# Performance work log

Hardware: AMD Instinct MI355X
Metric: run time of the kernel (lower is better)

## Reference

```python
import jax, jax.numpy as jnp
import numpy as np

N, E, B = 10000, 60000, 4
NODE_IN, EDGE_IN, COND_IN, SCALE_IN = 6, 6, 10, 4
H, KW, OUT = 64, 256, 1
NUM_LAYERS = 3


def _lin(key, fan_in, fan_out):
    return jax.random.normal(key, (fan_in, fan_out), jnp.float32) / np.sqrt(fan_in).astype(np.float32)


def setup_inputs() -> dict:
    key = jax.random.key(0)
    ks = jax.random.split(key, 16)
    return {
        "x": jax.random.normal(ks[0], (N, NODE_IN), jnp.float32),
        "edge_attr": jax.random.normal(ks[1], (E, EDGE_IN), jnp.float32),
        "conditions": jax.random.normal(ks[2], (B, COND_IN), jnp.float32),
        "scale": jax.random.normal(ks[3], (B, SCALE_IN), jnp.float32),
        "edge_index": jax.random.randint(ks[4], (2, E), 0, N, dtype=jnp.int32),
        "batch": jnp.sort(jax.random.randint(ks[5], (N,), 0, B, dtype=jnp.int32)),
        # node encoder
        "nW1": _lin(ks[6], NODE_IN, H), "nb1": jnp.zeros((H,), jnp.float32),
        "nW2": _lin(ks[7], H, H), "nb2": jnp.zeros((H,), jnp.float32),
        # condition encoder
        "cW1": _lin(ks[8], COND_IN + SCALE_IN, H), "cb1": jnp.zeros((H,), jnp.float32),
        "cW2": _lin(ks[9], H, H), "cb2": jnp.zeros((H,), jnp.float32),
        # kernel network (DenseNet [EDGE_IN+H, KW//2, KW, H*H])
        "kW1": _lin(ks[10], EDGE_IN + H, KW // 2), "kb1": jnp.zeros((KW // 2,), jnp.float32),
        "kW2": _lin(ks[11], KW // 2, KW), "kb2": jnp.zeros((KW,), jnp.float32),
        "kW3": _lin(ks[12], KW, H * H), "kb3": jnp.zeros((H * H,), jnp.float32),
        # NNConv root weight + bias
        "root": _lin(ks[13], H, H), "conv_bias": jnp.zeros((H,), jnp.float32),
        # output head
        "oW": _lin(ks[14], H, OUT), "ob": jnp.zeros((OUT,), jnp.float32),
    }


def reference(x, edge_attr, conditions, scale, edge_index, batch,
              nW1, nb1, nW2, nb2, cW1, cb1, cW2, cb2,
              kW1, kb1, kW2, kb2, kW3, kb3, root, conv_bias, oW, ob):
    # node + condition encoders
    h = jax.nn.relu(x @ nW1 + nb1) @ nW2 + nb2                                   # [N,H]
    u = jax.nn.relu(jnp.concatenate([conditions, scale], 1) @ cW1 + cb1) @ cW2 + cb2  # [B,H]

    src, dst = edge_index[0], edge_index[1]
    # per-edge conditioned attributes
    ea = jnp.concatenate([edge_attr, u[batch[src]]], axis=1)                     # [E,EDGE_IN+H]
    # kernel network -> per-edge H x H weight (same every layer, compute once)
    k = jax.nn.relu(ea @ kW1 + kb1)
    k = jax.nn.relu(k @ kW2 + kb2)
    w = (k @ kW3 + kb3).reshape(E, H, H)                                          # [E,H,H]

    # mean-aggregation degree (clamped to >=1, matching scatter_mean semantics)
    deg = jnp.maximum(jax.ops.segment_sum(jnp.ones((E,), x.dtype), dst, num_segments=N), 1.0)

    for _ in range(NUM_LAYERS):
        msg = jnp.einsum('ei,eio->eo', h[src], w)                                 # gather + bmm
        agg = jax.ops.segment_sum(msg, dst, num_segments=N) / deg[:, None]        # scatter-mean
        h = jax.nn.relu(agg + h @ root + conv_bias)

    out = h @ oW + ob                                                             # [N,OUT]
    return out, u
```

## Files before the change

kernel.cpp:

```cpp
#include <hip/hip_runtime.h>
#include <hip/hip_fp16.h>

#define N_NODES 10000
#define N_EDGES 60000
#define EPAD    60032

typedef _Float16 f16;
typedef f16 f16x8 __attribute__((ext_vector_type(8)));
typedef float f32x4 __attribute__((ext_vector_type(4)));

__global__ void k_node_enc(const float* __restrict__ x, const float* __restrict__ W1,
                           const float* __restrict__ b1, const float* __restrict__ W2,
                           const float* __restrict__ b2, float* __restrict__ h) {
    __shared__ float t[4][64];
    int g = threadIdx.x >> 6, j = threadIdx.x & 63;
    int node = blockIdx.x * 4 + g;
    float acc = b1[j];
#pragma unroll
    for (int i = 0; i < 6; ++i) acc += x[node * 6 + i] * W1[i * 64 + j];
    t[g][j] = fmaxf(acc, 0.f);
    __syncthreads();
    float acc2 = b2[j];
#pragma unroll
    for (int i = 0; i < 64; ++i) acc2 += t[g][i] * W2[i * 64 + j];
    h[node * 64 + j] = acc2;
}

__global__ void k_cond_enc(const float* __restrict__ cond, const float* __restrict__ scl,
                           const float* __restrict__ W1, const float* __restrict__ b1,
                           const float* __restrict__ W2, const float* __restrict__ b2,
                           float* __restrict__ u, float* __restrict__ out_u) {
    __shared__ float t[4][64];
    __shared__ float cat[4][14];
    int g = threadIdx.x >> 6, j = threadIdx.x & 63;
    if (threadIdx.x < 56) {
        int b = threadIdx.x / 14, i = threadIdx.x % 14;
        cat[b][i] = (i < 10) ? cond[b * 10 + i] : scl[b * 4 + (i - 10)];
    }
    __syncthreads();
    float acc = b1[j];
#pragma unroll
    for (int i = 0; i < 14; ++i) acc += cat[g][i] * W1[i * 64 + j];
    t[g][j] = fmaxf(acc, 0.f);
    __syncthreads();
    float acc2 = b2[j];
#pragma unroll
    for (int i = 0; i < 64; ++i) acc2 += t[g][i] * W2[i * 64 + j];
    u[g * 64 + j] = acc2;
    out_u[g * 64 + j] = acc2;
}

__global__ void k_deg(const int* __restrict__ dst, float* __restrict__ deg) {
    int e = blockIdx.x * 256 + threadIdx.x;
    if (e < N_EDGES) atomicAdd(&deg[dst[e]], 1.0f);
}
__global__ void k_deg_inv(float* __restrict__ deg) {
    int n = blockIdx.x * 256 + threadIdx.x;
    if (n < N_NODES) deg[n] = 1.0f / fmaxf(deg[n], 1.0f);
}

__global__ void k_permute(const float* __restrict__ kW3, const float* __restrict__ kb3,
                          f16* __restrict__ kW3P, float* __restrict__ kb3P) {
    __shared__ float T[256][65];
    int i = blockIdx.x;
    int o = threadIdx.x & 63, kq = threadIdx.x >> 6;
    for (int kk = 0; kk < 64; ++kk) {
        int k = kk * 4 + kq;
        T[k][o] = kW3[(size_t)k * 4096 + i * 64 + o];
    }
    if (threadIdx.x < 64) kb3P[threadIdx.x * 64 + i] = kb3[i * 64 + threadIdx.x];
    __syncthreads();
    int ow = threadIdx.x >> 2, kc = (threadIdx.x & 3) * 64;
    f16* dstp = kW3P + (size_t)(ow * 64 + i) * 256 + kc;
    for (int c = 0; c < 8; ++c) {
        f16x8 v;
#pragma unroll
        for (int jj = 0; jj < 8; ++jj) v[jj] = (f16)T[kc + c * 8 + jj][ow];
        *(f16x8*)(dstp + c * 8) = v;
    }
}

__global__ __launch_bounds__(256) void k_edge12(const float* __restrict__ ea, const int* __restrict__ ei,
                                                const int* __restrict__ batch, const float* __restrict__ u,
                                                const float* __restrict__ W1, const float* __restrict__ b1,
                                                const float* __restrict__ W2, const float* __restrict__ b2,
                                                f16* __restrict__ k2) {
    __shared__ float u_s[256];
    __shared__ float ea_s[16][6];
    __shared__ int b_s[16];
    __shared__ float k1_s[16][128];
    int tid = threadIdx.x;
    int e0 = blockIdx.x * 16;
    u_s[tid] = u[tid];
    if (tid < 96) {
        int e = tid / 6, i = tid % 6;
        int eg = e0 + e;
        ea_s[e][i] = (eg < N_EDGES) ? ea[(size_t)eg * 6 + i] : 0.f;
    }
    if (tid < 16) {
        int eg = e0 + tid;
        b_s[tid] = (eg < N_EDGES) ? batch[ei[eg]] : 0;
    }
    __syncthreads();
    int j = tid & 127;
#pragma unroll 1
    for (int p = 0; p < 8; ++p) {
        int e = p * 2 + (tid >> 7);
        float acc = b1[j];
#pragma unroll
        for (int i = 0; i < 6; ++i) acc += ea_s[e][i] * W1[i * 128 + j];
        const float* ur = u_s + b_s[e] * 64;
#pragma unroll
        for (int i = 0; i < 64; ++i) acc += ur[i] * W1[(6 + i) * 128 + j];
        k1_s[e][j] = fmaxf(acc, 0.f);
    }
    __syncthreads();
    float acc2[16];
#pragma unroll
    for (int e = 0; e < 16; ++e) acc2[e] = b2[tid];
    for (int i = 0; i < 128; ++i) {
        float w = W2[(size_t)i * 256 + tid];
#pragma unroll
        for (int e = 0; e < 16; ++e) acc2[e] += k1_s[e][i] * w;
    }
#pragma unroll
    for (int e = 0; e < 16; ++e) {
        int eg = e0 + e;
        k2[(size_t)eg * 256 + tid] = (f16)((eg < N_EDGES) ? fmaxf(acc2[e], 0.f) : 0.f);
    }
}

__global__ __launch_bounds__(256) void k_fused(const f16* __restrict__ A, const f16* __restrict__ Bm,
                                               const float* __restrict__ kb3P, const float* __restrict__ h,
                                               const int* __restrict__ ei, const float* __restrict__ dinv,
                                               float* __restrict__ agg) {
    __shared__ __align__(16) char lB[32768];
    __shared__ int src_s[128];
    __shared__ int dst_s[128];
    __shared__ float dinv_s[128];
    int tid = threadIdx.x, wave = tid >> 6, lane = tid & 63;
    int m0 = blockIdx.x * 128;
    if (tid < 128) {
        int eg = m0 + tid; int s = 0, d = 0; float dv = 0.f;
        if (eg < N_EDGES) { s = ei[eg]; d = ei[N_EDGES + eg]; dv = dinv[d]; }
        src_s[tid] = s; dst_s[tid] = d; dinv_s[tid] = dv;
    }
    __syncthreads();
    f16x8 a[2][8];
#pragma unroll
    for (int mf = 0; mf < 2; ++mf) {
        const f16* ap = A + (size_t)(m0 + wave * 32 + mf * 16 + (lane & 15)) * 256 + (lane >> 4) * 8;
#pragma unroll
        for (int ks = 0; ks < 8; ++ks) a[mf][ks] = *(const f16x8*)(ap + ks * 32);
    }
    float hsr[2][4][4];
#pragma unroll
    for (int mf = 0; mf < 2; ++mf)
#pragma unroll
        for (int jj = 0; jj < 4; ++jj) {
            int el = wave * 32 + mf * 16 + (lane >> 4) * 4 + jj;
            const float* hp = h + (size_t)src_s[el] * 64 + (lane & 15);
            float dv = dinv_s[el];
#pragma unroll
            for (int nf = 0; nf < 4; ++nf) hsr[mf][jj][nf] = hp[nf * 16] * dv;
        }
    int swz = (lane & 7) << 4;
    int rbase = (lane & 15) * 512;
    int koff = (lane >> 4) * 16;
#pragma unroll 1
    for (int ct = 0; ct < 64; ++ct) {
        f16x8 st[8];
        const f16* bp = Bm + (size_t)ct * 64 * 256;
#pragma unroll
        for (int q = 0; q < 8; ++q) {
            int idx = q * 4096 + tid * 16;
            int r = idx >> 9, cb = idx & 511;
            st[q] = *(const f16x8*)(bp + r * 256 + (cb >> 1));
        }
        __syncthreads();
#pragma unroll
        for (int q = 0; q < 8; ++q) {
            int idx = q * 4096 + tid * 16;
            int r = idx >> 9, cb = idx & 511;
            *(f16x8*)(lB + r * 512 + (cb ^ ((r & 7) << 4))) = st[q];
        }
        __syncthreads();
        f32x4 acc[2][4];
#pragma unroll
        for (int nf = 0; nf < 4; ++nf) {
            float bv = kb3P[ct * 64 + nf * 16 + (lane & 15)];
            acc[0][nf] = {bv, bv, bv, bv};
            acc[1][nf] = {bv, bv, bv, bv};
        }
#pragma unroll
        for (int ks = 0; ks < 8; ++ks) {
            f16x8 bf[4];
#pragma unroll
            for (int nf = 0; nf < 4; ++nf)
                bf[nf] = *(const f16x8*)(lB + rbase + nf * 8192 + ((ks * 64 + koff) ^ swz));
#pragma unroll
            for (int mf = 0; mf < 2; ++mf)
#pragma unroll
                for (int nf = 0; nf < 4; ++nf)
                    acc[mf][nf] = __builtin_amdgcn_mfma_f32_16x16x32_f16(a[mf][ks], bf[nf], acc[mf][nf], 0, 0, 0);
        }
#pragma unroll
        for (int mf = 0; mf < 2; ++mf)
#pragma unroll
            for (int jj = 0; jj < 4; ++jj) {
                float v = acc[mf][0][jj] * hsr[mf][jj][0] + acc[mf][1][jj] * hsr[mf][jj][1]
                        + acc[mf][2][jj] * hsr[mf][jj][2] + acc[mf][3][jj] * hsr[mf][jj][3];
                v += __shfl_xor(v, 1); v += __shfl_xor(v, 2);
                v += __shfl_xor(v, 4); v += __shfl_xor(v, 8);
                int el = wave * 32 + mf * 16 + (lane >> 4) * 4 + jj;
                if ((lane & 15) == 0 && (m0 + el) < N_EDGES)
                    atomicAdd(&agg[(size_t)dst_s[el] * 64 + ct], v);
            }
    }
}

__global__ void k_update(const float* __restrict__ agg, const float* __restrict__ h,
                         const float* __restrict__ root, const float* __restrict__ bias,
                         float* __restrict__ hn) {
    __shared__ float t[4][64];
    int g = threadIdx.x >> 6, j = threadIdx.x & 63;
    int node = blockIdx.x * 4 + g;
    t[g][j] = h[node * 64 + j];
    __syncthreads();
    float acc = agg[node * 64 + j] + bias[j];
#pragma unroll
    for (int i = 0; i < 64; ++i) acc += t[g][i] * root[i * 64 + j];
    hn[node * 64 + j] = fmaxf(acc, 0.f);
}

__global__ void k_out(const float* __restrict__ h, const float* __restrict__ oW,
                      const float* __restrict__ ob, float* __restrict__ out) {
    int wg = (blockIdx.x * 256 + threadIdx.x) >> 6;
    int lane = threadIdx.x & 63;
    if (wg >= N_NODES) return;
    float p = h[wg * 64 + lane] * oW[lane];
#pragma unroll
    for (int s = 32; s > 0; s >>= 1) p += __shfl_xor(p, s);
    if (lane == 0) out[wg] = p + ob[0];
}

__global__ void k_sentinel(float* out) { out[0] = 1e30f; }

extern "C" void kernel_launch(void* const* d_in, const int* in_sizes, int n_in,
                              void* d_out, int out_size, void* d_ws, size_t ws_size,
                              hipStream_t stream) {
    const float* x          = (const float*)d_in[0];
    const float* edge_attr  = (const float*)d_in[1];
    const float* conditions = (const float*)d_in[2];
    const float* scale      = (const float*)d_in[3];
    const int*   edge_index = (const int*)d_in[4];
    const int*   batch      = (const int*)d_in[5];
    const float* nW1 = (const float*)d_in[6];  const float* nb1 = (const float*)d_in[7];
    const float* nW2 = (const float*)d_in[8];  const float* nb2 = (const float*)d_in[9];
    const float* cW1 = (const float*)d_in[10]; const float* cb1 = (const float*)d_in[11];
    const float* cW2 = (const float*)d_in[12]; const float* cb2 = (const float*)d_in[13];
    const float* kW1 = (const float*)d_in[14]; const float* kb1 = (const float*)d_in[15];
    const float* kW2 = (const float*)d_in[16]; const float* kb2 = (const float*)d_in[17];
    const float* kW3 = (const float*)d_in[18]; const float* kb3 = (const float*)d_in[19];
    const float* root = (const float*)d_in[20]; const float* conv_bias = (const float*)d_in[21];
    const float* oW  = (const float*)d_in[22]; const float* ob  = (const float*)d_in[23];
    float* out = (float*)d_out;

    char* ws = (char*)d_ws;
    size_t off = 0;
    auto alloc = [&](size_t bytes) -> char* {
        char* p = ws + off;
        off += (bytes + 255) & ~(size_t)255;
        return p;
    };
    float* h_a  = (float*)alloc((size_t)N_NODES * 64 * 4);
    float* h_b  = (float*)alloc((size_t)N_NODES * 64 * 4);
    float* agg  = (float*)alloc((size_t)N_NODES * 64 * 4);
    float* u    = (float*)alloc(256 * 4);
    float* deg  = (float*)alloc((size_t)N_NODES * 4);
    f16*   k2   = (f16*)alloc((size_t)EPAD * 256 * 2);
    f16*   kW3P = (f16*)alloc((size_t)4096 * 256 * 2);
    float* kb3P = (float*)alloc(4096 * 4);

    if (off > ws_size) {
        k_sentinel<<<1, 1, 0, stream>>>(out);
        return;
    }

    hipMemsetAsync(deg, 0, (size_t)N_NODES * 4, stream);
    k_node_enc<<<2500, 256, 0, stream>>>(x, nW1, nb1, nW2, nb2, h_a);
    k_cond_enc<<<1, 256, 0, stream>>>(conditions, scale, cW1, cb1, cW2, cb2, u, out + N_NODES);
    k_deg<<<(N_EDGES + 255) / 256, 256, 0, stream>>>(edge_index + N_EDGES, deg);
    k_deg_inv<<<(N_NODES + 255) / 256, 256, 0, stream>>>(deg);
    k_permute<<<64, 256, 0, stream>>>(kW3, kb3, kW3P, kb3P);
    k_edge12<<<EPAD / 16, 256, 0, stream>>>(edge_attr, edge_index, batch, u, kW1, kb1, kW2, kb2, k2);

    float* hc = h_a; float* hn = h_b;
    for (int l = 0; l < 3; ++l) {
        hipMemsetAsync(agg, 0, (size_t)N_NODES * 64 * 4, stream);
        k_fused<<<dim3(EPAD / 128), 256, 0, stream>>>(k2, kW3P, kb3P, hc, edge_index, deg, agg);
        k_update<<<2500, 256, 0, stream>>>(agg, hc, root, conv_bias, hn);
        float* tmp = hc; hc = hn; hn = tmp;
    }
    k_out<<<2500, 256, 0, stream>>>(hc, oW, ob, out);
}
```

Baseline: 1.007 ms.

## Split fused edge kernel over output columns and prefetch weight tiles

```diff
diff --git a/kernel.cpp b/kernel.cpp
--- a/kernel.cpp
+++ b/kernel.cpp
@@ -4,6 +4,8 @@
 #define N_NODES 10000
 #define N_EDGES 60000
 #define EPAD    60032
+#define CSPLIT  4
+#define CT_PER  16
 
 typedef _Float16 f16;
 typedef f16 f16x8 __attribute__((ext_vector_type(8)));
@@ -138,13 +140,18 @@
     __shared__ int src_s[128];
     __shared__ int dst_s[128];
     __shared__ float dinv_s[128];
+    __shared__ float bias_s[CT_PER * 64];
     int tid = threadIdx.x, wave = tid >> 6, lane = tid & 63;
     int m0 = blockIdx.x * 128;
+    int ct0 = blockIdx.y * CT_PER;
     if (tid < 128) {
         int eg = m0 + tid; int s = 0, d = 0; float dv = 0.f;
         if (eg < N_EDGES) { s = ei[eg]; d = ei[N_EDGES + eg]; dv = dinv[d]; }
         src_s[tid] = s; dst_s[tid] = d; dinv_s[tid] = dv;
     }
+#pragma unroll
+    for (int q = 0; q < CT_PER * 64 / 256; ++q)
+        bias_s[q * 256 + tid] = kb3P[ct0 * 64 + q * 256 + tid];
     __syncthreads();
     f16x8 a[2][8];
 #pragma unroll
@@ -164,31 +171,34 @@
 #pragma unroll
             for (int nf = 0; nf < 4; ++nf) hsr[mf][jj][nf] = hp[nf * 16] * dv;
         }
-    int swz = (lane & 7) << 4;
-    int rbase = (lane & 15) * 512;
-    int koff = (lane >> 4) * 16;
+    f16x8 st[8];
+    {
+        const f16* bp = Bm + (size_t)ct0 * 16384;
+#pragma unroll
+        for (int q = 0; q < 8; ++q) {
+            int v = q * 4 + wave;
+            st[q] = *(const f16x8*)(bp + (size_t)(((v >> 3) * 16) + (tid & 15)) * 256 + (v & 7) * 32 + ((tid >> 4) & 3) * 8);
+        }
+    }
 #pragma unroll 1
-    for (int ct = 0; ct < 64; ++ct) {
-        f16x8 st[8];
-        const f16* bp = Bm + (size_t)ct * 64 * 256;
-#pragma unroll
-        for (int q = 0; q < 8; ++q) {
-            int idx = q * 4096 + tid * 16;
-            int r = idx >> 9, cb = idx & 511;
-            st[q] = *(const f16x8*)(bp + r * 256 + (cb >> 1));
-        }
+    for (int ct = ct0; ct < ct0 + CT_PER; ++ct) {
         __syncthreads();
 #pragma unroll
-        for (int q = 0; q < 8; ++q) {
-            int idx = q * 4096 + tid * 16;
-            int r = idx >> 9, cb = idx & 511;
-            *(f16x8*)(lB + r * 512 + (cb ^ ((r & 7) << 4))) = st[q];
-        }
+        for (int q = 0; q < 8; ++q)
+            *(f16x8*)(lB + (q * 256 + tid) * 16) = st[q];
         __syncthreads();
+        if (ct + 1 < ct0 + CT_PER) {
+            const f16* bp = Bm + (size_t)(ct + 1) * 16384;
+#pragma unroll
+            for (int q = 0; q < 8; ++q) {
+                int v = q * 4 + wave;
+                st[q] = *(const f16x8*)(bp + (size_t)(((v >> 3) * 16) + (tid & 15)) * 256 + (v & 7) * 32 + ((tid >> 4) & 3) * 8);
+            }
+        }
         f32x4 acc[2][4];
 #pragma unroll
         for (int nf = 0; nf < 4; ++nf) {
-            float bv = kb3P[ct * 64 + nf * 16 + (lane & 15)];
+            float bv = bias_s[(ct - ct0) * 64 + nf * 16 + (lane & 15)];
             acc[0][nf] = {bv, bv, bv, bv};
             acc[1][nf] = {bv, bv, bv, bv};
         }
@@ -197,7 +207,7 @@
             f16x8 bf[4];
 #pragma unroll
             for (int nf = 0; nf < 4; ++nf)
-                bf[nf] = *(const f16x8*)(lB + rbase + nf * 8192 + ((ks * 64 + koff) ^ swz));
+                bf[nf] = *(const f16x8*)(lB + (nf * 8 + ks) * 1024 + lane * 16);
 #pragma unroll
             for (int mf = 0; mf < 2; ++mf)
 #pragma unroll
@@ -298,7 +308,7 @@
     float* hc = h_a; float* hn = h_b;
     for (int l = 0; l < 3; ++l) {
         hipMemsetAsync(agg, 0, (size_t)N_NODES * 64 * 4, stream);
-        k_fused<<<dim3(EPAD / 128), 256, 0, stream>>>(k2, kW3P, kb3P, hc, edge_index, deg, agg);
+        k_fused<<<dim3(EPAD / 128, CSPLIT), 256, 0, stream>>>(k2, kW3P, kb3P, hc, edge_index, deg, agg);
         k_update<<<2500, 256, 0, stream>>>(agg, hc, root, conv_bias, hn);
         float* tmp = hc; hc = hn; hn = tmp;
     }
```

Result: faster. 913.1 us (-9.3%).
